# Kernel tuning notes

Measured on AMD Instinct MI355X. Metric: run time of the kernel, lower is better.

## Reference

```python
import jax, jax.numpy as jnp
import numpy as np

B = 8192
E = 8
H = 128
NUM_CLASSES = 3
SIM_THRESHOLD = 0.8
EFF_THRESHOLD = 0.1
TARGET_TEMP = 1.0
W_LB, W_EFF, W_CONS, W_ENT, W_TEMP = 0.1, 0.05, 0.1, 0.01, 0.01


def setup_inputs() -> dict:
    key = jax.random.key(0)
    k1, k2, k3, k4 = jax.random.split(key, 4)
    logits = jax.random.normal(k1, (B, NUM_CLASSES), dtype=jnp.float32)
    targets = jax.random.randint(k2, (B,), 0, NUM_CLASSES, dtype=jnp.int64)
    raw = jax.random.uniform(k3, (B, E), dtype=jnp.float32)
    routing_probs = raw / raw.sum(axis=-1, keepdims=True)  # rows sum to 1
    input_embeddings = jax.random.uniform(k4, (B, H), dtype=jnp.float32)
    temperature = jnp.ones((1,), dtype=jnp.float32)
    return {
        "logits": logits,
        "targets": targets,
        "routing_probs": routing_probs,
        "input_embeddings": input_embeddings,
        "temperature": temperature,
    }


def _dynamo_loss(logits, routing_probs, input_embeddings, temperature, targets):
    # --- task loss: cross entropy (sentiment) ---
    logp_cls = jax.nn.log_softmax(logits, axis=-1)
    task_loss = -jnp.take_along_axis(logp_cls, targets[:, None], axis=-1).mean()

    # --- load balance: var(mean usage) / (1/E)^2 (torch.var unbiased) ---
    expert_usage = routing_probs.mean(axis=0)  # [E]
    lb_loss = W_LB * jnp.var(expert_usage, ddof=1) * (E ** 2)

    # --- efficiency: sum of probs below threshold, averaged over batch ---
    small = jnp.where(routing_probs < EFF_THRESHOLD, routing_probs, 0.0)
    eff_loss = W_EFF * small.sum(axis=-1).mean()

    # --- consistency: masked pairwise KL over similar samples ---
    nrm = input_embeddings / jnp.linalg.norm(input_embeddings, axis=-1, keepdims=True)
    sim = nrm @ nrm.T  # [B, B]
    mask = (sim > SIM_THRESHOLD) & ~jnp.eye(B, dtype=bool)
    logp = jax.nn.log_softmax(routing_probs, axis=-1)  # [B, E]
    p = jnp.exp(logp)
    a = jnp.sum(p * logp, axis=-1)  # [B], sum_e p_j log p_j
    # KL(i,j) = sum_e p_j (log p_j - log p_i) = a[j] - logp[i] . p[j]
    kl = a[None, :] - logp @ p.T  # [B, B]
    num_pairs = mask.sum()
    kl_sum = jnp.sum(jnp.where(mask, kl, 0.0))
    cons_loss = W_CONS * jnp.where(num_pairs > 0, kl_sum / jnp.maximum(num_pairs, 1), 0.0)

    # --- entropy regularization (maximize entropy of routing_probs-as-probs) ---
    eps = 1e-8
    entropy = -jnp.sum(routing_probs * jnp.log(routing_probs + eps), axis=-1)
    ent_loss = W_ENT * (-entropy.mean())

    # --- temperature regularization ---
    temp_loss = W_TEMP * jnp.mean((temperature - TARGET_TEMP) ** 2)

    return task_loss + lb_loss + eff_loss + cons_loss + ent_loss + temp_loss


def reference(logits, targets, routing_probs, input_embeddings, temperature):
    return _dynamo_loss(logits, routing_probs, input_embeddings, temperature, targets)
```

## Files before the change

kernel.cpp:

```cpp
#include <hip/hip_runtime.h>
#include <stdint.h>

#define B_SZ 8192
#define LOG8 2.0794415416798357f
#define NTILE 2080

typedef __attribute__((ext_vector_type(8))) short short8;
typedef __attribute__((ext_vector_type(4))) float floatx4;

typedef __attribute__((address_space(1))) const uint4 guint4;
typedef __attribute__((address_space(3))) uint4 luint4;

__device__ inline void async_cp16(const uint4* g, uint4* l) {
    __builtin_amdgcn_global_load_lds((guint4*)g, (luint4*)l, 16, 0, 0);
}

__device__ inline unsigned short f2bf(float f) {
    unsigned int u = __float_as_uint(f);
    u = (u + 0x7FFFu + ((u >> 16) & 1u)) >> 16;
    return (unsigned short)u;
}
__device__ inline float bf2f(unsigned short s) {
    return __uint_as_float(((unsigned int)s) << 16);
}
__device__ inline float wredf(float x) {
#pragma unroll
    for (int o = 32; o; o >>= 1) x += __shfl_down(x, o);
    return x;
}
__device__ inline int wredi(int x) {
#pragma unroll
    for (int o = 32; o; o >>= 1) x += __shfl_down(x, o);
    return x;
}


__global__ __launch_bounds__(512) void prep_all(
    const float* __restrict__ logits,
    const int* __restrict__ targets,
    const float* __restrict__ routing,
    const float* __restrict__ emb,
    unsigned short* __restrict__ nrm,
    unsigned short* __restrict__ nlq,
    unsigned short* __restrict__ pb,
    float* __restrict__ aprime,
    float* __restrict__ prepslot) {
    __shared__ float pred[8][11];
    const int bid = blockIdx.x;
    const int lane = threadIdx.x & 63;
    const int wave = threadIdx.x >> 6;

    if (bid < 256) {
#pragma unroll
        for (int iter = 0; iter < 4; ++iter) {
            int row = (((iter << 8) + bid) << 3) + wave;
            const float2* e2 = (const float2*)(emb + (size_t)row * 128);
            float2 v = e2[lane];
            float ss = v.x * v.x + v.y * v.y;
            ss = wredf(ss);
            ss = __shfl(ss, 0);
            float inv = rsqrtf(ss);
            ushort2 o;
            o.x = f2bf(v.x * inv);
            o.y = f2bf(v.y * inv);
            ((ushort2*)(nrm + (size_t)row * 128))[lane] = o;
        }
        return;
    }

    int row = ((bid - 256) << 9) + threadIdx.x;

    const float4* r4 = (const float4*)(routing + (size_t)row * 8);
    float4 va = r4[0], vb = r4[1];
    float v[8] = {va.x, va.y, va.z, va.w, vb.x, vb.y, vb.z, vb.w};

    float mx = v[0];
#pragma unroll
    for (int e = 1; e < 8; ++e) mx = fmaxf(mx, v[e]);
    float ex[8], s = 0.f;
#pragma unroll
    for (int e = 0; e < 8; ++e) { ex[e] = expf(v[e] - mx); s += ex[e]; }
    float ls = logf(s);
    float inv_s = 1.f / s;

    union { unsigned short u[8]; uint4 q; } lu, pu;
    float ap = 0.f;
#pragma unroll
    for (int e = 0; e < 8; ++e) {
        unsigned short pe = f2bf(ex[e] * inv_s);
        unsigned short le = f2bf(v[e] - mx - ls + LOG8);
        pu.u[e] = pe;
        lu.u[e] = le ^ 0x8000;
        ap += bf2f(pe) * bf2f(le);
    }
    ((uint4*)nlq)[row] = lu.q;
    ((uint4*)pb)[row] = pu.q;
    aprime[row] = ap;

    float eff = 0.f, ent = 0.f;
#pragma unroll
    for (int e = 0; e < 8; ++e) {
        if (v[e] < 0.1f) eff += v[e];
        ent += v[e] * logf(v[e] + 1e-8f);
    }

    const float* lg = logits + (size_t)row * 3;
    float a0 = lg[0], a1 = lg[1], a2 = lg[2];
    float mm = fmaxf(a0, fmaxf(a1, a2));
    float lse = mm + logf(expf(a0 - mm) + expf(a1 - mm) + expf(a2 - mm));
    int tg = targets[row];
    float tv = (tg == 0) ? a0 : ((tg == 1) ? a1 : a2);
    float task = lse - tv;

    task = wredf(task);
    eff = wredf(eff);
    ent = wredf(ent);
    float cs[8];
#pragma unroll
    for (int e = 0; e < 8; ++e) cs[e] = wredf(v[e]);

    if (lane == 0) {
        pred[wave][0] = task;
        pred[wave][1] = eff;
        pred[wave][2] = ent;
#pragma unroll
        for (int e = 0; e < 8; ++e) pred[wave][3 + e] = cs[e];
    }
    __syncthreads();
    if (threadIdx.x < 11) {
        float s2 = 0.f;
#pragma unroll
        for (int w = 0; w < 8; ++w) s2 += pred[w][threadIdx.x];
        prepslot[(bid - 256) * 11 + threadIdx.x] = s2;
    }
}

__global__ __launch_bounds__(512, 4) void tile_sym(
    const unsigned short* __restrict__ nrm,
    const unsigned short* __restrict__ nlq,
    const unsigned short* __restrict__ pb,
    const float* __restrict__ aprime,
    float* __restrict__ klslot,
    unsigned int* __restrict__ cntslot) {
    __shared__ uint4 sh[4096];

    const int t = threadIdx.x;
    const int L = blockIdx.x;
    const int wave = t >> 6, lane = t & 63;

    int bi = (int)((129.0f - sqrtf((float)(16641 - 8 * L))) * 0.5f);
    int T = bi * 64 - ((bi * (bi - 1)) >> 1);
    while (L < T) { --bi; T = bi * 64 - ((bi * (bi - 1)) >> 1); }
    while (L >= T + (64 - bi)) { T += 64 - bi; ++bi; }
    const int bj = bi + (L - T);
    const bool diag = (bi == bj);
    const int iBase = bi << 7, jBase = bj << 7;

    const uint4* n4 = (const uint4*)nrm;
    const int s0 = t & 7, r0 = t >> 3;
    const int s1 = (t + 512) & 7, r1 = (t + 512) >> 3;
    const int g0 = s0 ^ (r0 & 7), g1 = s1 ^ (r1 & 7);

    async_cp16(&n4[((size_t)(iBase + r0) << 4) + g0], sh + (wave << 6));
    async_cp16(&n4[((size_t)(iBase + r1) << 4) + g1], sh + 512 + (wave << 6));
    async_cp16(&n4[((size_t)(jBase + r0) << 4) + g0], sh + 1024 + (wave << 6));
    async_cp16(&n4[((size_t)(jBase + r1) << 4) + g1], sh + 1536 + (wave << 6));

    __syncthreads();

    async_cp16(&n4[((size_t)(iBase + r0) << 4) + 8 + g0], sh + 2048 + (wave << 6));
    async_cp16(&n4[((size_t)(iBase + r1) << 4) + 8 + g1], sh + 2560 + (wave << 6));
    async_cp16(&n4[((size_t)(jBase + r0) << 4) + 8 + g0], sh + 3072 + (wave << 6));
    async_cp16(&n4[((size_t)(jBase + r1) << 4) + 8 + g1], sh + 3584 + (wave << 6));

    const int wr = wave >> 2, wc = wave & 3;
    const int m = lane & 15, q = lane >> 4;
    const short8 zero8 = (short8){0, 0, 0, 0, 0, 0, 0, 0};

    short8 crA[4], crB[2];
#pragma unroll
    for (int a = 0; a < 4; ++a) {
        int ri = iBase + (wr << 6) + (a << 4) + m;
        short8 v = zero8;
        if (q == 0) v = *(const short8*)&nlq[(size_t)ri << 3];
        else if (q == 1) { if (!diag) v = *(const short8*)&pb[(size_t)ri << 3]; }
        else if (q == 2) {
            v[1] = (short)0x3F80;
            if (!diag) v[0] = (short)f2bf(aprime[ri]);
        }
        crA[a] = v;
    }
#pragma unroll
    for (int b = 0; b < 2; ++b) {
        int cj = jBase + (wc << 5) + (b << 4) + m;
        short8 v = zero8;
        if (q == 0) v = *(const short8*)&pb[(size_t)cj << 3];
        else if (q == 1) v = *(const short8*)&nlq[(size_t)cj << 3];
        else if (q == 2) {
            v[0] = (short)0x3F80;
            v[1] = (short)f2bf(aprime[cj]);
        }
        crB[b] = v;
    }

    floatx4 simacc[4][2];
#pragma unroll
    for (int a = 0; a < 4; ++a)
#pragma unroll
        for (int b = 0; b < 2; ++b) simacc[a][b] = (floatx4){0.f, 0.f, 0.f, 0.f};

    const int m7 = m & 7;
    const int raOff = (wr << 6) << 3;
    const int rbOff = (wc << 5) << 3;

#pragma unroll
    for (int ks = 0; ks < 2; ++ks) {
        const int sg = ((ks << 2) + q) ^ m7;
        short8 af[4], bfr[2];
#pragma unroll
        for (int a = 0; a < 4; ++a)
            af[a] = *(const short8*)(sh + raOff + (((a << 4) + m) << 3) + sg);
#pragma unroll
        for (int b = 0; b < 2; ++b)
            bfr[b] = *(const short8*)(sh + 1024 + rbOff + (((b << 4) + m) << 3) + sg);
#pragma unroll
        for (int a = 0; a < 4; ++a)
#pragma unroll
            for (int b = 0; b < 2; ++b)
                simacc[a][b] = __builtin_amdgcn_mfma_f32_16x16x32_bf16(
                    af[a], bfr[b], simacc[a][b], 0, 0, 0);
    }

    __syncthreads();

#pragma unroll
    for (int ks = 0; ks < 2; ++ks) {
        const int sg = ((ks << 2) + q) ^ m7;
        short8 af[4], bfr[2];
#pragma unroll
        for (int a = 0; a < 4; ++a)
            af[a] = *(const short8*)(sh + 2048 + raOff + (((a << 4) + m) << 3) + sg);
#pragma unroll
        for (int b = 0; b < 2; ++b)
            bfr[b] = *(const short8*)(sh + 3072 + rbOff + (((b << 4) + m) << 3) + sg);
#pragma unroll
        for (int a = 0; a < 4; ++a)
#pragma unroll
            for (int b = 0; b < 2; ++b)
                simacc[a][b] = __builtin_amdgcn_mfma_f32_16x16x32_bf16(
                    af[a], bfr[b], simacc[a][b], 0, 0, 0);
    }

    float klLocal = 0.f;
    int cntLocal = 0;
#pragma unroll
    for (int a = 0; a < 4; ++a) {
        const int gRow0 = iBase + (wr << 6) + (a << 4) + (q << 2);
#pragma unroll
        for (int b = 0; b < 2; ++b) {
            const int gCol = jBase + (wc << 5) + (b << 4) + m;
            floatx4 cr = __builtin_amdgcn_mfma_f32_16x16x32_bf16(
                crA[a], crB[b], (floatx4){0.f, 0.f, 0.f, 0.f}, 0, 0, 0);
            if (diag) {
#pragma unroll
                for (int r = 0; r < 4; ++r) {
                    if ((simacc[a][b][r] > 0.8f) && (gRow0 + r != gCol)) {
                        klLocal += cr[r];
                        cntLocal += 1;
                    }
                }
            } else {
#pragma unroll
                for (int r = 0; r < 4; ++r) {
                    if (simacc[a][b][r] > 0.8f) {
                        klLocal += cr[r];
                        cntLocal += 2;
                    }
                }
            }
        }
    }

    klLocal = wredf(klLocal);
    cntLocal = wredi(cntLocal);

    __syncthreads();
    float* redk = (float*)sh;
    int* redc = (int*)(redk + 8);
    if (lane == 0) { redk[wave] = klLocal; redc[wave] = cntLocal; }
    __syncthreads();

    if (t == 0) {
        float k = 0.f;
        int c = 0;
#pragma unroll
        for (int w = 0; w < 8; ++w) { k += redk[w]; c += redc[w]; }
        klslot[L] = k;
        cntslot[L] = (unsigned int)c;
    }
}

__global__ void finalize_k(const float* __restrict__ klslot,
                           const unsigned int* __restrict__ cntslot,
                           const float* __restrict__ prepslot,
                           const float* __restrict__ temp,
                           float* __restrict__ out) {
    __shared__ float sk[4];
    __shared__ int sc[4];
    __shared__ float sp[11];
    const int t = threadIdx.x, lane = t & 63, wave = t >> 6;

    float k = 0.f;
    int c = 0;
    for (int i = t; i < NTILE; i += 256) { k += klslot[i]; c += (int)cntslot[i]; }
    k = wredf(k);
    c = wredi(c);
    if (lane == 0) { sk[wave] = k; sc[wave] = c; }
    if (t < 11) {
        float s = 0.f;
        for (int r = 0; r < 16; ++r) s += prepslot[r * 11 + t];
        sp[t] = s;
    }
    __syncthreads();
    if (t == 0) {
        float K = sk[0] + sk[1] + sk[2] + sk[3];
        int C = sc[0] + sc[1] + sc[2] + sc[3];
        const float invB = 1.f / (float)B_SZ;
        float task = sp[0] * invB;
        float eff = 0.05f * sp[1] * invB;
        float entl = 0.01f * sp[2] * invB;
        float cons = 0.1f * (C > 0 ? K / (float)C : 0.f);
        float u[8], mean = 0.f;
        for (int e = 0; e < 8; ++e) { u[e] = sp[3 + e] * invB; mean += u[e]; }
        mean *= 0.125f;
        float var = 0.f;
        for (int e = 0; e < 8; ++e) { float d = u[e] - mean; var += d * d; }
        var *= (1.f / 7.f);
        float lb = 0.1f * var * 64.f;
        float tt = temp[0] - 1.f;
        out[0] = task + lb + eff + cons + entl + 0.01f * tt * tt;
    }
}

extern "C" void kernel_launch(void* const* d_in, const int* in_sizes, int n_in,
                              void* d_out, int out_size, void* d_ws, size_t ws_size,
                              hipStream_t stream) {
    const float* logits = (const float*)d_in[0];
    const int* targets = (const int*)d_in[1];
    const float* routing = (const float*)d_in[2];
    const float* emb = (const float*)d_in[3];
    const float* temp = (const float*)d_in[4];

    char* ws = (char*)d_ws;
    unsigned short* nrm = (unsigned short*)ws;
    unsigned short* nlq = (unsigned short*)(ws + 2097152);
    unsigned short* pb = (unsigned short*)(ws + 2228224);
    float* aprime = (float*)(ws + 2359296);
    float* klslot = (float*)(ws + 2392064);
    unsigned int* cntslot = (unsigned int*)(ws + 2400384);
    float* prepslot = (float*)(ws + 2408704);

    prep_all<<<272, 512, 0, stream>>>(logits, targets, routing, emb,
                                      nrm, nlq, pb, aprime, prepslot);
    tile_sym<<<NTILE, 512, 0, stream>>>(nrm, nlq, pb, aprime, klslot, cntslot);
    finalize_k<<<1, 256, 0, stream>>>(klslot, cntslot, prepslot, temp,
                                      (float*)d_out);
}
```

Measured before the change: 103.5 us.

## Fuse finalize into tile kernel via last-block atomic reduction

The separate finalize kernel is removed. Each tile block atomically adds its KL sum and pair count to global totals and bumps a done counter, and the last block to finish reduces the per-block prep statistics and writes the loss. The prep kernel is also restructured so every block normalizes embeddings and then uses one wave for 32 routing rows. This removes one kernel launch, but adds global atomics on a single address and makes the float KL sum order nondeterministic.

```diff
diff --git a/kernel.cpp b/kernel.cpp
--- a/kernel.cpp
+++ b/kernel.cpp
@@ -44,73 +44,85 @@
     unsigned short* __restrict__ nlq,
     unsigned short* __restrict__ pb,
     float* __restrict__ aprime,
-    float* __restrict__ prepslot) {
-    __shared__ float pred[8][11];
+    float* __restrict__ prepslot,
+    float* __restrict__ klT,
+    unsigned int* __restrict__ cntT,
+    unsigned int* __restrict__ doneCnt) {
     const int bid = blockIdx.x;
     const int lane = threadIdx.x & 63;
     const int wave = threadIdx.x >> 6;
 
-    if (bid < 256) {
-#pragma unroll
-        for (int iter = 0; iter < 4; ++iter) {
-            int row = (((iter << 8) + bid) << 3) + wave;
-            const float2* e2 = (const float2*)(emb + (size_t)row * 128);
-            float2 v = e2[lane];
-            float ss = v.x * v.x + v.y * v.y;
-            ss = wredf(ss);
-            ss = __shfl(ss, 0);
-            float inv = rsqrtf(ss);
-            ushort2 o;
-            o.x = f2bf(v.x * inv);
-            o.y = f2bf(v.y * inv);
-            ((ushort2*)(nrm + (size_t)row * 128))[lane] = o;
-        }
-        return;
-    }
-
-    int row = ((bid - 256) << 9) + threadIdx.x;
-
-    const float4* r4 = (const float4*)(routing + (size_t)row * 8);
-    float4 va = r4[0], vb = r4[1];
-    float v[8] = {va.x, va.y, va.z, va.w, vb.x, vb.y, vb.z, vb.w};
-
-    float mx = v[0];
-#pragma unroll
-    for (int e = 1; e < 8; ++e) mx = fmaxf(mx, v[e]);
-    float ex[8], s = 0.f;
-#pragma unroll
-    for (int e = 0; e < 8; ++e) { ex[e] = expf(v[e] - mx); s += ex[e]; }
-    float ls = logf(s);
-    float inv_s = 1.f / s;
-
-    union { unsigned short u[8]; uint4 q; } lu, pu;
-    float ap = 0.f;
-#pragma unroll
-    for (int e = 0; e < 8; ++e) {
-        unsigned short pe = f2bf(ex[e] * inv_s);
-        unsigned short le = f2bf(v[e] - mx - ls + LOG8);
-        pu.u[e] = pe;
-        lu.u[e] = le ^ 0x8000;
-        ap += bf2f(pe) * bf2f(le);
-    }
-    ((uint4*)nlq)[row] = lu.q;
-    ((uint4*)pb)[row] = pu.q;
-    aprime[row] = ap;
-
-    float eff = 0.f, ent = 0.f;
-#pragma unroll
-    for (int e = 0; e < 8; ++e) {
-        if (v[e] < 0.1f) eff += v[e];
-        ent += v[e] * logf(v[e] + 1e-8f);
-    }
-
-    const float* lg = logits + (size_t)row * 3;
-    float a0 = lg[0], a1 = lg[1], a2 = lg[2];
-    float mm = fmaxf(a0, fmaxf(a1, a2));
-    float lse = mm + logf(expf(a0 - mm) + expf(a1 - mm) + expf(a2 - mm));
-    int tg = targets[row];
-    float tv = (tg == 0) ? a0 : ((tg == 1) ? a1 : a2);
-    float task = lse - tv;
+    if (bid == 0 && threadIdx.x == 0) {
+        *klT = 0.f;
+        *cntT = 0u;
+        *doneCnt = 0u;
+    }
+
+#pragma unroll
+    for (int iter = 0; iter < 4; ++iter) {
+        int row = (((iter << 8) + bid) << 3) + wave;
+        const float2* e2 = (const float2*)(emb + (size_t)row * 128);
+        float2 vv = e2[lane];
+        float ss = vv.x * vv.x + vv.y * vv.y;
+        ss = wredf(ss);
+        ss = __shfl(ss, 0);
+        float inv = rsqrtf(ss);
+        ushort2 o;
+        o.x = f2bf(vv.x * inv);
+        o.y = f2bf(vv.y * inv);
+        ((ushort2*)(nrm + (size_t)row * 128))[lane] = o;
+    }
+
+    if (wave != 0) return;
+
+    float task = 0.f, eff = 0.f, ent = 0.f;
+    float v[8] = {0.f, 0.f, 0.f, 0.f, 0.f, 0.f, 0.f, 0.f};
+
+    if (lane < 32) {
+        int row = (bid << 5) + lane;
+
+        const float4* r4 = (const float4*)(routing + (size_t)row * 8);
+        float4 va = r4[0], vb = r4[1];
+        v[0] = va.x; v[1] = va.y; v[2] = va.z; v[3] = va.w;
+        v[4] = vb.x; v[5] = vb.y; v[6] = vb.z; v[7] = vb.w;
+
+        float mx = v[0];
+#pragma unroll
+        for (int e = 1; e < 8; ++e) mx = fmaxf(mx, v[e]);
+        float ex[8], s = 0.f;
+#pragma unroll
+        for (int e = 0; e < 8; ++e) { ex[e] = expf(v[e] - mx); s += ex[e]; }
+        float ls = logf(s);
+        float inv_s = 1.f / s;
+
+        union { unsigned short u[8]; uint4 q; } lu, pu;
+        float ap = 0.f;
+#pragma unroll
+        for (int e = 0; e < 8; ++e) {
+            unsigned short pe = f2bf(ex[e] * inv_s);
+            unsigned short le = f2bf(v[e] - mx - ls + LOG8);
+            pu.u[e] = pe;
+            lu.u[e] = le ^ 0x8000;
+            ap += bf2f(pe) * bf2f(le);
+        }
+        ((uint4*)nlq)[row] = lu.q;
+        ((uint4*)pb)[row] = pu.q;
+        aprime[row] = ap;
+
+#pragma unroll
+        for (int e = 0; e < 8; ++e) {
+            if (v[e] < 0.1f) eff += v[e];
+            ent += v[e] * logf(v[e] + 1e-8f);
+        }
+
+        const float* lg = logits + (size_t)row * 3;
+        float a0 = lg[0], a1 = lg[1], a2 = lg[2];
+        float mm = fmaxf(a0, fmaxf(a1, a2));
+        float lse = mm + logf(expf(a0 - mm) + expf(a1 - mm) + expf(a2 - mm));
+        int tg = targets[row];
+        float tv = (tg == 0) ? a0 : ((tg == 1) ? a1 : a2);
+        task = lse - tv;
+    }
 
     task = wredf(task);
     eff = wredf(eff);
@@ -120,18 +132,12 @@
     for (int e = 0; e < 8; ++e) cs[e] = wredf(v[e]);
 
     if (lane == 0) {
-        pred[wave][0] = task;
-        pred[wave][1] = eff;
-        pred[wave][2] = ent;
-#pragma unroll
-        for (int e = 0; e < 8; ++e) pred[wave][3 + e] = cs[e];
-    }
-    __syncthreads();
-    if (threadIdx.x < 11) {
-        float s2 = 0.f;
-#pragma unroll
-        for (int w = 0; w < 8; ++w) s2 += pred[w][threadIdx.x];
-        prepslot[(bid - 256) * 11 + threadIdx.x] = s2;
+        float* ps = prepslot + bid * 11;
+        ps[0] = task;
+        ps[1] = eff;
+        ps[2] = ent;
+#pragma unroll
+        for (int e = 0; e < 8; ++e) ps[3 + e] = cs[e];
     }
 }
 
@@ -140,8 +146,12 @@
     const unsigned short* __restrict__ nlq,
     const unsigned short* __restrict__ pb,
     const float* __restrict__ aprime,
-    float* __restrict__ klslot,
-    unsigned int* __restrict__ cntslot) {
+    const float* __restrict__ prepslot,
+    const float* __restrict__ temp,
+    float* __restrict__ klT,
+    unsigned int* __restrict__ cntT,
+    unsigned int* __restrict__ doneCnt,
+    float* __restrict__ out) {
     __shared__ uint4 sh[4096];
 
     const int t = threadIdx.x;
@@ -286,54 +296,61 @@
 
     __syncthreads();
     float* redk = (float*)sh;
-    int* redc = (int*)(redk + 8);
-    if (lane == 0) { redk[wave] = klLocal; redc[wave] = cntLocal; }
+    int* redi_ = (int*)sh;
+    if (lane == 0) { redk[wave] = klLocal; redi_[8 + wave] = cntLocal; }
     __syncthreads();
 
     if (t == 0) {
         float k = 0.f;
         int c = 0;
 #pragma unroll
-        for (int w = 0; w < 8; ++w) { k += redk[w]; c += redc[w]; }
-        klslot[L] = k;
-        cntslot[L] = (unsigned int)c;
-    }
-}
-
-__global__ void finalize_k(const float* __restrict__ klslot,
-                           const unsigned int* __restrict__ cntslot,
-                           const float* __restrict__ prepslot,
-                           const float* __restrict__ temp,
-                           float* __restrict__ out) {
-    __shared__ float sk[4];
-    __shared__ int sc[4];
-    __shared__ float sp[11];
-    const int t = threadIdx.x, lane = t & 63, wave = t >> 6;
-
-    float k = 0.f;
-    int c = 0;
-    for (int i = t; i < NTILE; i += 256) { k += klslot[i]; c += (int)cntslot[i]; }
-    k = wredf(k);
-    c = wredi(c);
-    if (lane == 0) { sk[wave] = k; sc[wave] = c; }
-    if (t < 11) {
-        float s = 0.f;
-        for (int r = 0; r < 16; ++r) s += prepslot[r * 11 + t];
-        sp[t] = s;
-    }
-    __syncthreads();
+        for (int w = 0; w < 8; ++w) { k += redk[w]; c += redi_[8 + w]; }
+        atomicAdd(klT, k);
+        atomicAdd(cntT, (unsigned int)c);
+        __threadfence();
+        unsigned int old = atomicAdd(doneCnt, 1u);
+        redi_[16] = (old == (unsigned int)(NTILE - 1)) ? 1 : 0;
+    }
+    __syncthreads();
+    if (redi_[16] == 0) return;
+
+    float* sstat = (float*)sh;
+    if (t < 11) sstat[t] = 0.f;
+
+    float sv[11];
+    if (t < 256) {
+        const float* ps = prepslot + t * 11;
+#pragma unroll
+        for (int j = 0; j < 11; ++j) sv[j] = ps[j];
+    } else {
+#pragma unroll
+        for (int j = 0; j < 11; ++j) sv[j] = 0.f;
+    }
+#pragma unroll
+    for (int j = 0; j < 11; ++j) sv[j] = wredf(sv[j]);
+
+    __syncthreads();
+    if (lane == 0) {
+#pragma unroll
+        for (int j = 0; j < 11; ++j) atomicAdd(&sstat[j], sv[j]);
+    }
+    __syncthreads();
+
     if (t == 0) {
-        float K = sk[0] + sk[1] + sk[2] + sk[3];
-        int C = sc[0] + sc[1] + sc[2] + sc[3];
+        __threadfence();
+        float K = atomicAdd(klT, 0.f);
+        unsigned int C = atomicAdd(cntT, 0u);
         const float invB = 1.f / (float)B_SZ;
-        float task = sp[0] * invB;
-        float eff = 0.05f * sp[1] * invB;
-        float entl = 0.01f * sp[2] * invB;
-        float cons = 0.1f * (C > 0 ? K / (float)C : 0.f);
+        float task = sstat[0] * invB;
+        float eff = 0.05f * sstat[1] * invB;
+        float entl = 0.01f * sstat[2] * invB;
+        float cons = 0.1f * (C > 0u ? K / (float)C : 0.f);
         float u[8], mean = 0.f;
-        for (int e = 0; e < 8; ++e) { u[e] = sp[3 + e] * invB; mean += u[e]; }
+#pragma unroll
+        for (int e = 0; e < 8; ++e) { u[e] = sstat[3 + e] * invB; mean += u[e]; }
         mean *= 0.125f;
         float var = 0.f;
+#pragma unroll
         for (int e = 0; e < 8; ++e) { float d = u[e] - mean; var += d * d; }
         var *= (1.f / 7.f);
         float lb = 0.1f * var * 64.f;
@@ -356,13 +373,14 @@
     unsigned short* nlq = (unsigned short*)(ws + 2097152);
     unsigned short* pb = (unsigned short*)(ws + 2228224);
     float* aprime = (float*)(ws + 2359296);
-    float* klslot = (float*)(ws + 2392064);
-    unsigned int* cntslot = (unsigned int*)(ws + 2400384);
-    float* prepslot = (float*)(ws + 2408704);
-
-    prep_all<<<272, 512, 0, stream>>>(logits, targets, routing, emb,
-                                      nrm, nlq, pb, aprime, prepslot);
-    tile_sym<<<NTILE, 512, 0, stream>>>(nrm, nlq, pb, aprime, klslot, cntslot);
-    finalize_k<<<1, 256, 0, stream>>>(klslot, cntslot, prepslot, temp,
-                                      (float*)d_out);
-}
+    float* prepslot = (float*)(ws + 2392064);
+    float* klT = (float*)(ws + 2403328);
+    unsigned int* cntT = (unsigned int*)(ws + 2403332);
+    unsigned int* doneCnt = (unsigned int*)(ws + 2403336);
+
+    prep_all<<<256, 512, 0, stream>>>(logits, targets, routing, emb,
+                                      nrm, nlq, pb, aprime, prepslot,
+                                      klT, cntT, doneCnt);
+    tile_sym<<<NTILE, 512, 0, stream>>>(nrm, nlq, pb, aprime, prepslot, temp,
+                                        klT, cntT, doneCnt, (float*)d_out);
+}
```

Result: slower. 159.5 us (+54.2%).

## Halve tile LDS to raise occupancy and merge prep blocks

Applied to the files above, without the earlier changes.

The tile kernel now reuses one 32KB LDS buffer for both K-halves, loading the second half only after the first half's MFMAs finish, instead of staging both halves in 64KB. Launch bounds rise to 8 blocks per CU so more tiles can be resident. The prep kernel drops its 16 separate routing blocks: each of the 256 embedding blocks has wave 0 handle 32 routing rows, and finalize reduces 256 partial slots with wave reductions. The cost is that the second global load is serialized behind the first compute phase, with an extra barrier, and register pressure is capped tighter.

```diff
diff --git a/kernel.cpp b/kernel.cpp
--- a/kernel.cpp
+++ b/kernel.cpp
@@ -45,72 +45,75 @@
     unsigned short* __restrict__ pb,
     float* __restrict__ aprime,
     float* __restrict__ prepslot) {
-    __shared__ float pred[8][11];
     const int bid = blockIdx.x;
     const int lane = threadIdx.x & 63;
     const int wave = threadIdx.x >> 6;
 
-    if (bid < 256) {
-#pragma unroll
-        for (int iter = 0; iter < 4; ++iter) {
-            int row = (((iter << 8) + bid) << 3) + wave;
-            const float2* e2 = (const float2*)(emb + (size_t)row * 128);
-            float2 v = e2[lane];
-            float ss = v.x * v.x + v.y * v.y;
-            ss = wredf(ss);
-            ss = __shfl(ss, 0);
-            float inv = rsqrtf(ss);
-            ushort2 o;
-            o.x = f2bf(v.x * inv);
-            o.y = f2bf(v.y * inv);
-            ((ushort2*)(nrm + (size_t)row * 128))[lane] = o;
-        }
-        return;
-    }
-
-    int row = ((bid - 256) << 9) + threadIdx.x;
-
-    const float4* r4 = (const float4*)(routing + (size_t)row * 8);
-    float4 va = r4[0], vb = r4[1];
-    float v[8] = {va.x, va.y, va.z, va.w, vb.x, vb.y, vb.z, vb.w};
-
-    float mx = v[0];
-#pragma unroll
-    for (int e = 1; e < 8; ++e) mx = fmaxf(mx, v[e]);
-    float ex[8], s = 0.f;
-#pragma unroll
-    for (int e = 0; e < 8; ++e) { ex[e] = expf(v[e] - mx); s += ex[e]; }
-    float ls = logf(s);
-    float inv_s = 1.f / s;
-
-    union { unsigned short u[8]; uint4 q; } lu, pu;
-    float ap = 0.f;
-#pragma unroll
-    for (int e = 0; e < 8; ++e) {
-        unsigned short pe = f2bf(ex[e] * inv_s);
-        unsigned short le = f2bf(v[e] - mx - ls + LOG8);
-        pu.u[e] = pe;
-        lu.u[e] = le ^ 0x8000;
-        ap += bf2f(pe) * bf2f(le);
-    }
-    ((uint4*)nlq)[row] = lu.q;
-    ((uint4*)pb)[row] = pu.q;
-    aprime[row] = ap;
-
-    float eff = 0.f, ent = 0.f;
-#pragma unroll
-    for (int e = 0; e < 8; ++e) {
-        if (v[e] < 0.1f) eff += v[e];
-        ent += v[e] * logf(v[e] + 1e-8f);
-    }
-
-    const float* lg = logits + (size_t)row * 3;
-    float a0 = lg[0], a1 = lg[1], a2 = lg[2];
-    float mm = fmaxf(a0, fmaxf(a1, a2));
-    float lse = mm + logf(expf(a0 - mm) + expf(a1 - mm) + expf(a2 - mm));
-    int tg = targets[row];
-    float tv = (tg == 0) ? a0 : ((tg == 1) ? a1 : a2);
-    float task = lse - tv;
+#pragma unroll
+    for (int iter = 0; iter < 4; ++iter) {
+        int row = (((iter << 8) + bid) << 3) + wave;
+        const float2* e2 = (const float2*)(emb + (size_t)row * 128);
+        float2 vv = e2[lane];
+        float ss = vv.x * vv.x + vv.y * vv.y;
+        ss = wredf(ss);
+        ss = __shfl(ss, 0);
+        float inv = rsqrtf(ss);
+        ushort2 o;
+        o.x = f2bf(vv.x * inv);
+        o.y = f2bf(vv.y * inv);
+        ((ushort2*)(nrm + (size_t)row * 128))[lane] = o;
+    }
+
+    if (wave != 0) return;
+
+    float task = 0.f, eff = 0.f, ent = 0.f;
+    float v[8] = {0.f, 0.f, 0.f, 0.f, 0.f, 0.f, 0.f, 0.f};
+
+    if (lane < 32) {
+        int row = (bid << 5) + lane;
+
+        const float4* r4 = (const float4*)(routing + (size_t)row * 8);
+        float4 va = r4[0], vb = r4[1];
+        v[0] = va.x; v[1] = va.y; v[2] = va.z; v[3] = va.w;
+        v[4] = vb.x; v[5] = vb.y; v[6] = vb.z; v[7] = vb.w;
+
+        float mx = v[0];
+#pragma unroll
+        for (int e = 1; e < 8; ++e) mx = fmaxf(mx, v[e]);
+        float ex[8], s = 0.f;
+#pragma unroll
+        for (int e = 0; e < 8; ++e) { ex[e] = expf(v[e] - mx); s += ex[e]; }
+        float ls = logf(s);
+        float inv_s = 1.f / s;
+
+        union { unsigned short u[8]; uint4 q; } lu, pu;
+        float ap = 0.f;
+#pragma unroll
+        for (int e = 0; e < 8; ++e) {
+            unsigned short pe = f2bf(ex[e] * inv_s);
+            unsigned short le = f2bf(v[e] - mx - ls + LOG8);
+            pu.u[e] = pe;
+            lu.u[e] = le ^ 0x8000;
+            ap += bf2f(pe) * bf2f(le);
+        }
+        ((uint4*)nlq)[row] = lu.q;
+        ((uint4*)pb)[row] = pu.q;
+        aprime[row] = ap;
+
+#pragma unroll
+        for (int e = 0; e < 8; ++e) {
+            if (v[e] < 0.1f) eff += v[e];
+            ent += v[e] * logf(v[e] + 1e-8f);
+        }
+
+        const float* lg = logits + (size_t)row * 3;
+        float a0 = lg[0], a1 = lg[1], a2 = lg[2];
+        float mm = fmaxf(a0, fmaxf(a1, a2));
+        float lse = mm + logf(expf(a0 - mm) + expf(a1 - mm) + expf(a2 - mm));
+        int tg = targets[row];
+        float tv = (tg == 0) ? a0 : ((tg == 1) ? a1 : a2);
+        task = lse - tv;
+    }
 
     task = wredf(task);
     eff = wredf(eff);
@@ -120,29 +123,23 @@
     for (int e = 0; e < 8; ++e) cs[e] = wredf(v[e]);
 
     if (lane == 0) {
-        pred[wave][0] = task;
-        pred[wave][1] = eff;
-        pred[wave][2] = ent;
-#pragma unroll
-        for (int e = 0; e < 8; ++e) pred[wave][3 + e] = cs[e];
-    }
-    __syncthreads();
-    if (threadIdx.x < 11) {
-        float s2 = 0.f;
-#pragma unroll
-        for (int w = 0; w < 8; ++w) s2 += pred[w][threadIdx.x];
-        prepslot[(bid - 256) * 11 + threadIdx.x] = s2;
-    }
-}
-
-__global__ __launch_bounds__(512, 4) void tile_sym(
+        float* ps = prepslot + bid * 11;
+        ps[0] = task;
+        ps[1] = eff;
+        ps[2] = ent;
+#pragma unroll
+        for (int e = 0; e < 8; ++e) ps[3 + e] = cs[e];
+    }
+}
+
+__global__ __launch_bounds__(512, 8) void tile_sym(
     const unsigned short* __restrict__ nrm,
     const unsigned short* __restrict__ nlq,
     const unsigned short* __restrict__ pb,
     const float* __restrict__ aprime,
     float* __restrict__ klslot,
     unsigned int* __restrict__ cntslot) {
-    __shared__ uint4 sh[4096];
+    __shared__ uint4 sh[2048];
 
     const int t = threadIdx.x;
     const int L = blockIdx.x;
@@ -165,13 +162,6 @@
     async_cp16(&n4[((size_t)(iBase + r1) << 4) + g1], sh + 512 + (wave << 6));
     async_cp16(&n4[((size_t)(jBase + r0) << 4) + g0], sh + 1024 + (wave << 6));
     async_cp16(&n4[((size_t)(jBase + r1) << 4) + g1], sh + 1536 + (wave << 6));
-
-    __syncthreads();
-
-    async_cp16(&n4[((size_t)(iBase + r0) << 4) + 8 + g0], sh + 2048 + (wave << 6));
-    async_cp16(&n4[((size_t)(iBase + r1) << 4) + 8 + g1], sh + 2560 + (wave << 6));
-    async_cp16(&n4[((size_t)(jBase + r0) << 4) + 8 + g0], sh + 3072 + (wave << 6));
-    async_cp16(&n4[((size_t)(jBase + r1) << 4) + 8 + g1], sh + 3584 + (wave << 6));
 
     const int wr = wave >> 2, wc = wave & 3;
     const int m = lane & 15, q = lane >> 4;
@@ -213,6 +203,8 @@
     const int raOff = (wr << 6) << 3;
     const int rbOff = (wc << 5) << 3;
 
+    __syncthreads();
+
 #pragma unroll
     for (int ks = 0; ks < 2; ++ks) {
         const int sg = ((ks << 2) + q) ^ m7;
@@ -233,16 +225,23 @@
 
     __syncthreads();
 
+    async_cp16(&n4[((size_t)(iBase + r0) << 4) + 8 + g0], sh + (wave << 6));
+    async_cp16(&n4[((size_t)(iBase + r1) << 4) + 8 + g1], sh + 512 + (wave << 6));
+    async_cp16(&n4[((size_t)(jBase + r0) << 4) + 8 + g0], sh + 1024 + (wave << 6));
+    async_cp16(&n4[((size_t)(jBase + r1) << 4) + 8 + g1], sh + 1536 + (wave << 6));
+
+    __syncthreads();
+
 #pragma unroll
     for (int ks = 0; ks < 2; ++ks) {
         const int sg = ((ks << 2) + q) ^ m7;
         short8 af[4], bfr[2];
 #pragma unroll
         for (int a = 0; a < 4; ++a)
-            af[a] = *(const short8*)(sh + 2048 + raOff + (((a << 4) + m) << 3) + sg);
+            af[a] = *(const short8*)(sh + raOff + (((a << 4) + m) << 3) + sg);
 #pragma unroll
         for (int b = 0; b < 2; ++b)
-            bfr[b] = *(const short8*)(sh + 3072 + rbOff + (((b << 4) + m) << 3) + sg);
+            bfr[b] = *(const short8*)(sh + 1024 + rbOff + (((b << 4) + m) << 3) + sg);
 #pragma unroll
         for (int a = 0; a < 4; ++a)
 #pragma unroll
@@ -307,7 +306,7 @@
                            float* __restrict__ out) {
     __shared__ float sk[4];
     __shared__ int sc[4];
-    __shared__ float sp[11];
+    __shared__ float sp[4][11];
     const int t = threadIdx.x, lane = t & 63, wave = t >> 6;
 
     float k = 0.f;
@@ -316,24 +315,37 @@
     k = wredf(k);
     c = wredi(c);
     if (lane == 0) { sk[wave] = k; sc[wave] = c; }
-    if (t < 11) {
-        float s = 0.f;
-        for (int r = 0; r < 16; ++r) s += prepslot[r * 11 + t];
-        sp[t] = s;
-    }
-    __syncthreads();
+
+    float sv[11];
+    const float* ps = prepslot + t * 11;
+#pragma unroll
+    for (int j = 0; j < 11; ++j) sv[j] = ps[j];
+#pragma unroll
+    for (int j = 0; j < 11; ++j) sv[j] = wredf(sv[j]);
+    if (lane == 0) {
+#pragma unroll
+        for (int j = 0; j < 11; ++j) sp[wave][j] = sv[j];
+    }
+    __syncthreads();
+
     if (t == 0) {
         float K = sk[0] + sk[1] + sk[2] + sk[3];
         int C = sc[0] + sc[1] + sc[2] + sc[3];
+        float st[11];
+#pragma unroll
+        for (int j = 0; j < 11; ++j)
+            st[j] = sp[0][j] + sp[1][j] + sp[2][j] + sp[3][j];
         const float invB = 1.f / (float)B_SZ;
-        float task = sp[0] * invB;
-        float eff = 0.05f * sp[1] * invB;
-        float entl = 0.01f * sp[2] * invB;
+        float task = st[0] * invB;
+        float eff = 0.05f * st[1] * invB;
+        float entl = 0.01f * st[2] * invB;
         float cons = 0.1f * (C > 0 ? K / (float)C : 0.f);
         float u[8], mean = 0.f;
-        for (int e = 0; e < 8; ++e) { u[e] = sp[3 + e] * invB; mean += u[e]; }
+#pragma unroll
+        for (int e = 0; e < 8; ++e) { u[e] = st[3 + e] * invB; mean += u[e]; }
         mean *= 0.125f;
         float var = 0.f;
+#pragma unroll
         for (int e = 0; e < 8; ++e) { float d = u[e] - mean; var += d * d; }
         var *= (1.f / 7.f);
         float lb = 0.1f * var * 64.f;
@@ -360,7 +372,7 @@
     unsigned int* cntslot = (unsigned int*)(ws + 2400384);
     float* prepslot = (float*)(ws + 2408704);
 
-    prep_all<<<272, 512, 0, stream>>>(logits, targets, routing, emb,
+    prep_all<<<256, 512, 0, stream>>>(logits, targets, routing, emb,
                                       nrm, nlq, pb, aprime, prepslot);
     tile_sym<<<NTILE, 512, 0, stream>>>(nrm, nlq, pb, aprime, klslot, cntslot);
     finalize_k<<<1, 256, 0, stream>>>(klslot, cntslot, prepslot, temp,
```

Result: slower. 155.6 us (+50.4%).
